# Kernel optimization log

Hardware: AMD Instinct MI355X
Metric: run time of the kernel (lower is better)

The kernel has to match this reference:

```python
import jax, jax.numpy as jnp
from jax import lax
import numpy as np

B, T = 64, 256
PH, POSD, DEPD, DISTD, SDPD = 768, 32, 32, 32, 16
LH, TH, NUM_LABELS = 256, 256, 10
FEAT = PH + POSD + DEPD + 2 * DISTD + SDPD  # 912
TREE_IN = 2 * LH + DEPD                      # 544
D_ITERS = 9  # depth of heads[t]=t//2 tree is 8; 9 sweeps = exact recursion


def setup_inputs() -> dict:
    key = jax.random.key(0)
    ks = jax.random.split(key, 30)
    s = 0.05
    inp = {
        'token_features': jax.random.normal(ks[0], (B, T, PH), jnp.float32),
        'pos_ids': jax.random.randint(ks[1], (B, T), 0, 50),
        'dep_ids': jax.random.randint(ks[2], (B, T), 0, 40),
        'e1_idx': jax.random.randint(ks[3], (B,), 0, T),
        'e2_idx': jax.random.randint(ks[4], (B,), 0, T),
        'sdp_pos': jax.random.randint(ks[5], (B, T), 0, 3),
        'dep_heads': jnp.broadcast_to(jnp.arange(T) // 2, (B, T)),  # root=0 self-loop
        'root_idx': jnp.zeros((B,), jnp.int32),
        # embedding tables
        'pos_table': jax.random.normal(ks[6], (50, POSD)) * s,
        'dep_table': jax.random.normal(ks[7], (40, DEPD)) * s,
        'dist_table': jax.random.normal(ks[8], (21, DISTD)) * s,
        'sdp_table': jax.random.normal(ks[9], (3, SDPD)) * s,
        # feature transform
        'W_ft': jax.random.normal(ks[10], (FEAT, 512)) * s,
        'b_ft': jnp.zeros((512,), jnp.float32),
        # BiLSTM (torch gate order i,f,g,o)
        'Wih_f': jax.random.normal(ks[11], (512, 4 * LH)) * s,
        'Whh_f': jax.random.normal(ks[12], (LH, 4 * LH)) * s,
        'bl_f': jnp.zeros((4 * LH,), jnp.float32),
        'Wih_b': jax.random.normal(ks[13], (512, 4 * LH)) * s,
        'Whh_b': jax.random.normal(ks[14], (LH, 4 * LH)) * s,
        'bl_b': jnp.zeros((4 * LH,), jnp.float32),
        # child-sum TreeLSTM
        'W_iou': jax.random.normal(ks[15], (TREE_IN, 3 * TH)) * s,
        'U_iou': jax.random.normal(ks[16], (TH, 3 * TH)) * s,
        'b_iou': jnp.zeros((3 * TH,), jnp.float32),
        'Wf_t': jax.random.normal(ks[17], (TREE_IN, TH)) * s,
        'Uf_t': jax.random.normal(ks[18], (TH, TH)) * s,
        'bf_t': jnp.zeros((TH,), jnp.float32),
        # classifier
        'W1': jax.random.normal(ks[19], (TH, 256)) * s,
        'b1': jnp.zeros((256,), jnp.float32),
        'W2': jax.random.normal(ks[20], (256, NUM_LABELS)) * s,
        'b2': jnp.zeros((NUM_LABELS,), jnp.float32),
    }
    return inp


def _lstm_dir(x, Wih, Whh, b):
    xW = x @ Wih + b  # [B,T,4H]
    def step(carry, xt):
        h, c = carry
        g = xt + h @ Whh
        i, f, gg, o = jnp.split(g, 4, -1)
        c = jax.nn.sigmoid(f) * c + jax.nn.sigmoid(i) * jnp.tanh(gg)
        h = jax.nn.sigmoid(o) * jnp.tanh(c)
        return (h, c), h
    z = jnp.zeros((x.shape[0], LH), x.dtype)
    _, hs = lax.scan(step, (z, z), jnp.swapaxes(xW, 0, 1))
    return jnp.swapaxes(hs, 0, 1)


def _forward(token_features, pos_table, dep_table, dist_table, sdp_table,
             W_ft, b_ft, Wih_f, Whh_f, bl_f, Wih_b, Whh_b, bl_b,
             W_iou, U_iou, b_iou, Wf_t, Uf_t, bf_t, W1, b1, W2, b2,
             pos_ids, dep_ids, e1_idx, e2_idx, sdp_pos, dep_heads, root_idx):
    pos_emb = pos_table[pos_ids]
    dep_emb = dep_table[dep_ids]
    pos_range = jnp.arange(T)[None, :]
    d1 = jnp.clip(pos_range - e1_idx[:, None] + 10, 0, 20)  # bucket_distance
    d2 = jnp.clip(pos_range - e2_idx[:, None] + 10, 0, 20)
    combined = jnp.concatenate(
        [token_features, pos_emb, dep_emb, dist_table[d1], dist_table[d2], sdp_table[sdp_pos]], -1)
    transformed = jnp.tanh(combined @ W_ft + b_ft)  # [B,T,512] (dropout=eval identity)
    h_f = _lstm_dir(transformed, Wih_f, Whh_f, bl_f)
    h_b = _lstm_dir(transformed[:, ::-1], Wih_b, Whh_b, bl_b)[:, ::-1]
    seq_out = jnp.concatenate([h_f, h_b], -1)           # [B,T,512]
    x_tree = jnp.concatenate([seq_out, dep_emb], -1)    # [B,T,544]
    seg = (dep_heads + jnp.arange(B)[:, None] * T).reshape(-1)
    mask = (dep_heads != pos_range).astype(x_tree.dtype)[..., None]  # drop root self-loop
    xWiou = x_tree @ W_iou + b_iou
    xWf = x_tree @ Wf_t + bf_t
    xWf_par = jnp.take_along_axis(xWf, dep_heads[..., None], axis=1)  # parent's Wf x at each child

    def seg_sum(v):
        return jax.ops.segment_sum(v.reshape(B * T, TH), seg, num_segments=B * T).reshape(B, T, TH)

    def step(carry, _):
        h, c = carry
        h_sum = seg_sum(h * mask)                       # sum of children hidden
        f = jax.nn.sigmoid(xWf_par + h @ Uf_t)          # per-child forget gate
        fc = seg_sum(f * c * mask)
        i, o, u = jnp.split(xWiou + h_sum @ U_iou, 3, -1)
        c2 = jax.nn.sigmoid(i) * jnp.tanh(u) + fc
        h2 = jax.nn.sigmoid(o) * jnp.tanh(c2)
        return (h2, c2), None

    z = jnp.zeros((B, T, TH), x_tree.dtype)
    (h, _), _ = lax.scan(step, (z, z), None, length=D_ITERS)
    root_h = h[jnp.arange(B), root_idx]
    logits = jax.nn.relu(root_h @ W1 + b1) @ W2 + b2
    return logits


def reference(token_features, pos_ids, dep_ids, e1_idx, e2_idx, sdp_pos, dep_heads, root_idx,
              pos_table, dep_table, dist_table, sdp_table, W_ft, b_ft,
              Wih_f, Whh_f, bl_f, Wih_b, Whh_b, bl_b,
              W_iou, U_iou, b_iou, Wf_t, Uf_t, bf_t, W1, b1, W2, b2):
    return _forward(token_features, pos_table, dep_table, dist_table, sdp_table,
                    W_ft, b_ft, Wih_f, Whh_f, bl_f, Wih_b, Whh_b, bl_b,
                    W_iou, U_iou, b_iou, Wf_t, Uf_t, bf_t, W1, b1, W2, b2,
                    pos_ids, dep_ids, e1_idx, e2_idx, sdp_pos, dep_heads, root_idx)
```

## Files before the change

kernel.cpp:

```cpp
#include <hip/hip_runtime.h>
#include <hip/hip_fp16.h>
#include <math.h>


typedef _Float16 f16x8 __attribute__((ext_vector_type(8)));
typedef float    f32x4 __attribute__((ext_vector_type(4)));

union PK1 { _Float16 h; unsigned short u16; };

#define LOG2E 1.44269504088896340736f

__device__ __forceinline__ float fexp2(float x) {
  return __builtin_amdgcn_exp2f(x);
}
__device__ __forceinline__ float frcp(float x) {
  return __builtin_amdgcn_rcpf(x);
}
__device__ __forceinline__ float sigm(float x) {
  return frcp(1.0f + fexp2(-LOG2E * x));
}
__device__ __forceinline__ float tanh_fast(float x) {
  return 1.0f - 2.0f * frcp(1.0f + fexp2(2.0f * LOG2E * x));
}

struct EmbArgs {
  const float* tf; const int* pos_ids; const int* dep_ids;
  const int* e1; const int* e2; const int* sdp;
  const float* pos_tab; const float* dep_tab; const float* dist_tab;
  const float* sdp_tab;
};

__global__ __launch_bounds__(256) void k_prep(
    const float* __restrict__ W_ft, __half* __restrict__ BTft,
    const float* __restrict__ Wih_f, __half* __restrict__ BTwhf,
    const float* __restrict__ Wih_b, __half* __restrict__ BTwhb,
    const float* __restrict__ W_iou, __half* __restrict__ BTiou,
    const float* __restrict__ Wf_t, __half* __restrict__ BTf,
    const float* __restrict__ Whh_f, __half* __restrict__ WBf,
    const float* __restrict__ Whh_b, __half* __restrict__ WBb,
    unsigned int* __restrict__ FLG,
    const int* __restrict__ dep_ids, const float* __restrict__ dep_tab,
    __half* __restrict__ XT,
    const float* __restrict__ Uf, __half* __restrict__ BTuf,
    const float* __restrict__ Uiou, __half* __restrict__ BTuiou) {
  int e = blockIdx.x * 256 + threadIdx.x;
  if (e < 466944) {
    int n = e & 511, k = e >> 9;
    BTft[(size_t)n * 928 + k] = __float2half_rn(W_ft[(size_t)k * 512 + n]);
  } else if ((e -= 466944) < 8192) {
    int n = e >> 4, kk = e & 15;
    BTft[(size_t)n * 928 + 912 + kk] = __float2half_rn(0.0f);
  } else if ((e -= 8192) < 524288) {
    int n = e & 1023, k = e >> 10;
    BTwhf[(size_t)n * 512 + k] = __float2half_rn(Wih_f[(size_t)k * 1024 + n]);
  } else if ((e -= 524288) < 524288) {
    int n = e & 1023, k = e >> 10;
    BTwhb[(size_t)n * 512 + k] = __float2half_rn(Wih_b[(size_t)k * 1024 + n]);
  } else if ((e -= 524288) < 417792) {
    int n = e % 768, k = e / 768;
    BTiou[(size_t)n * 544 + k] = __float2half_rn(W_iou[(size_t)k * 768 + n]);
  } else if ((e -= 417792) < 139264) {
    int n = e & 255, k = e >> 8;
    BTf[(size_t)n * 544 + k] = __float2half_rn(Wf_t[(size_t)k * 256 + n]);
  } else if ((e -= 139264) < 262144) {
    int k = e & 255, c = (e >> 8) & 127, j = e >> 15;
    int col = (c & 3) * 256 + j * 32 + (c >> 2);
    WBf[e] = __float2half_rn(Whh_f[(size_t)k * 1024 + col]);
  } else if ((e -= 262144) < 262144) {
    int k = e & 255, c = (e >> 8) & 127, j = e >> 15;
    int col = (c & 3) * 256 + j * 32 + (c >> 2);
    WBb[e] = __float2half_rn(Whh_b[(size_t)k * 1024 + col]);
  } else if ((e -= 262144) < 32768) {
    FLG[e] = 0u;
  } else if ((e -= 32768) < 524288) {
    int row = e >> 5, kk = e & 31;
    XT[(size_t)row * 544 + 512 + kk] =
        __float2half_rn(dep_tab[dep_ids[row] * 32 + kk]);
  } else if ((e -= 524288) < 65536) {
    int n = e & 255, k = e >> 8;
    BTuf[(size_t)n * 256 + k] = __float2half_rn(Uf[(size_t)k * 256 + n]);
  } else {
    e -= 65536;
    int n = e % 768, k = e / 768;
    BTuiou[(size_t)n * 256 + k] = __float2half_rn(Uiou[(size_t)k * 768 + n]);
  }
}

__global__ __launch_bounds__(256) void k_mgemm(
    const __half* __restrict__ A16, const __half* __restrict__ BT,
    const float* __restrict__ bias, void* __restrict__ out,
    int N, int K, int lda, int a_embed, int act_tanh, int out_mode,
    EmbArgs ea,
    const __half* __restrict__ BT2, const float* __restrict__ bias2,
    void* __restrict__ out2, int N2, int split_bx) {
  __shared__ _Float16 As[128 * 40];
  __shared__ _Float16 Bs[128 * 40];
  int tid = threadIdx.x;
  int lane = tid & 63, wave = tid >> 6;
  int wm = wave & 1, wn = wave >> 1;
  int bxx = blockIdx.x;
  const __half* BTp = BT; const float* biasp = bias;
  void* outp = out; int Np = N;
  if (bxx >= split_bx) {
    bxx -= split_bx; BTp = BT2; biasp = bias2; outp = out2; Np = N2;
  }
  int col0 = bxx * 128, row0 = blockIdx.y * 128;

  f32x4 acc[4][4];
#pragma unroll
  for (int i = 0; i < 4; ++i)
#pragma unroll
    for (int j = 0; j < 4; ++j) acc[i][j] = (f32x4)0.0f;

  for (int kt = 0; kt < K; kt += 32) {
    __syncthreads();
#pragma unroll
    for (int it = 0; it < 2; ++it) {
      int lin = tid + it * 256;
      int r = lin & 127, kh8 = (lin >> 7) * 8;
      f16x8 va;
      if (!a_embed) {
        va = *(const f16x8*)(A16 + (size_t)(row0 + r) * lda + kt + kh8);
      } else {
        int row = row0 + r;
        int k0 = kt + kh8;
        if (k0 >= 912) {
          va = (f16x8)(_Float16)0.0f;
        } else {
          const float* src;
          if (k0 < 768) {
            src = ea.tf + (size_t)row * 768 + k0;
          } else {
            int b_ = row >> 8, t_ = row & 255;
            if (k0 < 800) src = ea.pos_tab + ea.pos_ids[row] * 32 + (k0 - 768);
            else if (k0 < 832) src = ea.dep_tab + ea.dep_ids[row] * 32 + (k0 - 800);
            else if (k0 < 864) {
              int d = t_ - ea.e1[b_] + 10; d = d < 0 ? 0 : (d > 20 ? 20 : d);
              src = ea.dist_tab + d * 32 + (k0 - 832);
            } else if (k0 < 896) {
              int d = t_ - ea.e2[b_] + 10; d = d < 0 ? 0 : (d > 20 ? 20 : d);
              src = ea.dist_tab + d * 32 + (k0 - 864);
            } else {
              src = ea.sdp_tab + ea.sdp[row] * 16 + (k0 - 896);
            }
          }
          float4 a = *(const float4*)src;
          float4 b2 = *(const float4*)(src + 4);
          va[0] = (_Float16)a.x;  va[1] = (_Float16)a.y;
          va[2] = (_Float16)a.z;  va[3] = (_Float16)a.w;
          va[4] = (_Float16)b2.x; va[5] = (_Float16)b2.y;
          va[6] = (_Float16)b2.z; va[7] = (_Float16)b2.w;
        }
      }
      *(f16x8*)&As[r * 40 + kh8] = va;
      f16x8 vb = *(const f16x8*)(BTp + (size_t)(col0 + r) * K + kt + kh8);
      *(f16x8*)&Bs[r * 40 + kh8] = vb;
    }
    __syncthreads();
    f16x8 af[4], bf[4];
    int kq = (lane >> 4) * 8;
#pragma unroll
    for (int mt = 0; mt < 4; ++mt)
      af[mt] = *(const f16x8*)&As[(wm * 64 + mt * 16 + (lane & 15)) * 40 + kq];
#pragma unroll
    for (int nt = 0; nt < 4; ++nt)
      bf[nt] = *(const f16x8*)&Bs[(wn * 64 + nt * 16 + (lane & 15)) * 40 + kq];
#pragma unroll
    for (int mt = 0; mt < 4; ++mt)
#pragma unroll
      for (int nt = 0; nt < 4; ++nt)
        acc[mt][nt] = __builtin_amdgcn_mfma_f32_16x16x32_f16(
            af[mt], bf[nt], acc[mt][nt], 0, 0, 0);
  }

#pragma unroll
  for (int mt = 0; mt < 4; ++mt) {
#pragma unroll
    for (int nt = 0; nt < 4; ++nt) {
      int col = col0 + wn * 64 + nt * 16 + (lane & 15);
      float bv = biasp[col];
#pragma unroll
      for (int r = 0; r < 4; ++r) {
        int row = row0 + wm * 64 + mt * 16 + (lane >> 4) * 4 + r;
        float v = acc[mt][nt][r] + bv;
        if (act_tanh) v = tanh_fast(v);
        if (out_mode == 0) {
          ((float*)outp)[(size_t)row * Np + col] = v;
        } else if (out_mode == 1) {
          ((__half*)outp)[(size_t)row * Np + col] = __float2half_rn(v);
        } else {
          int b_ = row >> 8, t_ = row & 255;
          int g_ = col >> 8, u_ = col & 255;
          int sl = u_ >> 5, ul = u_ & 31;
          ((__half*)outp)[((((size_t)(t_ * 8 + sl) * 4 + g_) * 64 + b_) * 32) + ul] =
              __float2half_rn(v);
        }
      }
    }
  }
}

__global__ __launch_bounds__(256, 1) void k_lstm6(
    const __half* __restrict__ XFs, const __half* __restrict__ XBs,
    const __half* __restrict__ WBf, const __half* __restrict__ WBb,
    __half* __restrict__ HexS, unsigned int* __restrict__ flags,
    __half* __restrict__ XT) {
  int bx = blockIdx.x;
  int dir = bx >> 6, slice = (bx >> 2) & 15, bq = bx & 3;
  int tid = threadIdx.x;
  int lane = tid & 63, wave = tid >> 6;
  const __half* xWs = dir ? XBs : XFs;
  const __half* WB = dir ? WBb : WBf;
  __half* hexd = HexS + (size_t)dir * 256 * 16384;
  unsigned int* flg = flags + (dir * 4 + bq) * 4096;

  __shared__ _Float16 H[16 * 266];
  __shared__ float GT[16 * 69];

  f16x8 bfrag[8];
  {
    int c = (slice & 1) * 64 + wave * 16 + (lane & 15);
#pragma unroll
    for (int kt = 0; kt < 8; ++kt)
      bfrag[kt] = *(const f16x8*)(
          WB + ((size_t)((slice >> 1) * 128 + c) * 256) + kt * 32 +
          (lane >> 4) * 8);
  }
  for (int i = tid; i < 16 * 266 / 8; i += 256)
    ((f16x8*)H)[i] = (f16x8)(_Float16)0.0f;
  float cst = 0.0f;
  int b_own = tid >> 4;
  int uc = tid & 15;
  int bglob = bq * 16 + b_own;
  size_t xw_off = bglob * 32 + (slice & 1) * 16 + uc;
  float xwg[4];
  {
    int t0 = dir ? 255 : 0;
    const __half* xwp = xWs + ((size_t)(t0 * 8 + (slice >> 1)) * 8192) + xw_off;
#pragma unroll
    for (int g = 0; g < 4; ++g) xwg[g] = __half2float(xwp[g * 2048]);
  }
  __syncthreads();

  for (int s = 0; s < 256; ++s) {
    int t = dir ? (255 - s) : s;

    f32x4 acc = (f32x4)0.0f;
#pragma unroll
    for (int kt = 0; kt < 8; ++kt) {
      f16x8 a = *(const f16x8*)&H[(lane & 15) * 266 + kt * 32 +
                                  (lane >> 4) * 8];
      acc = __builtin_amdgcn_mfma_f32_16x16x32_f16(a, bfrag[kt], acc, 0, 0, 0);
    }
    __syncthreads();
    {
      int col = wave * 16 + (lane & 15);
#pragma unroll
      for (int r = 0; r < 4; ++r) {
        int b = (lane >> 4) * 4 + r;
        GT[b * 69 + col] = acc[r];
      }
    }
    __syncthreads();
    float4 g4 = *(const float4*)&GT[b_own * 69 + 4 * uc];
    float gi = g4.x + xwg[0];
    float gf = g4.y + xwg[1];
    float gg = g4.z + xwg[2];
    float go = g4.w + xwg[3];
    cst = sigm(gf) * cst + sigm(gi) * tanh_fast(gg);
    float hn = sigm(go) * tanh_fast(cst);
    PK1 hv; hv.h = (_Float16)hn;
    H[b_own * 266 + slice * 16 + uc] = hv.h;

    if (s < 255) {
      __half* hexq = hexd + (size_t)s * 16384;
      unsigned short* dst =
          (unsigned short*)(hexq + (bq * 16 + slice) * 256 + tid);
      __hip_atomic_store(dst, hv.u16, __ATOMIC_RELAXED,
                         __HIP_MEMORY_SCOPE_AGENT);
      asm volatile("s_waitcnt vmcnt(0)" ::: "memory");
      __syncthreads();
      if (tid == 0)
        __hip_atomic_store(&flg[(slice << 8) + s], 1u, __ATOMIC_RELAXED,
                           __HIP_MEMORY_SCOPE_AGENT);
      XT[(size_t)((bglob << 8) + t) * 544 + dir * 256 + slice * 16 + uc] =
          *(__half*)&hv.h;
      float xwn[4];
      {
        int tn = dir ? (254 - s) : (s + 1);
        const __half* xwp =
            xWs + ((size_t)(tn * 8 + (slice >> 1)) * 8192) + xw_off;
#pragma unroll
        for (int g = 0; g < 4; ++g) xwn[g] = __half2float(xwp[g * 2048]);
      }
      if (tid < 16 && tid != slice) {
        while (__hip_atomic_load(&flg[(tid << 8) + s], __ATOMIC_RELAXED,
                                 __HIP_MEMORY_SCOPE_AGENT) == 0u) {}
      }
      __syncthreads();
#pragma unroll
      for (int i = 0; i < 15; ++i) {
        int ps = i + (i >= slice ? 1 : 0);
        __half pv = hexq[(bq * 16 + ps) * 256 + tid];
        H[b_own * 266 + ps * 16 + uc] = *(_Float16*)&pv;
      }
      __syncthreads();
#pragma unroll
      for (int g = 0; g < 4; ++g) xwg[g] = xwn[g];
    } else {
      XT[(size_t)((bglob << 8) + t) * 544 + dir * 256 + slice * 16 + uc] =
          *(__half*)&hv.h;
    }
  }
}

__global__ __launch_bounds__(256) void k_tgemm(
    const float* __restrict__ A,
    const __half* __restrict__ BT0, float* __restrict__ Cv0, int M0,
    int band_lo0, int blog0,
    const __half* __restrict__ BT1, float* __restrict__ Cv1, int M1,
    int band_lo1, int blog1, int nb0,
    const int* __restrict__ dep_heads,
    const float* __restrict__ xWf, const float* __restrict__ c_buf) {
  __shared__ _Float16 As[128 * 40];
  __shared__ _Float16 Bs[128 * 40];
  int tid = threadIdx.x;
  int lane = tid & 63, wave = tid >> 6;
  int wm = wave & 1, wn = wave >> 1;
  int f = blockIdx.x;
  const __half* BT; float* Cv; int M, N, band_lo, blog, amode, epi;
  int bx, by;
  if (f < nb0) {
    BT = BT0; Cv = Cv0; M = M0; N = 256; band_lo = band_lo0; blog = blog0;
    amode = 1; epi = 2; bx = f & 1; by = f >> 1;
  } else {
    f -= nb0;
    BT = BT1; Cv = Cv1; M = M1; N = 768; band_lo = band_lo1; blog = blog1;
    amode = 2; epi = 0; bx = f % 6; by = f / 6;
  }
  int col0 = bx * 128, row0 = by * 128;
  int bmask = (1 << blog) - 1;

  f32x4 acc[4][4];
#pragma unroll
  for (int i = 0; i < 4; ++i)
#pragma unroll
    for (int j = 0; j < 4; ++j) acc[i][j] = (f32x4)0.0f;

  for (int kt = 0; kt < 256; kt += 32) {
    __syncthreads();
#pragma unroll
    for (int it = 0; it < 2; ++it) {
      int lin = tid + it * 256;
      int r = lin & 127, kh8 = (lin >> 7) * 8;
      int row = row0 + r;
      f16x8 va = (f16x8)(_Float16)0.0f;
      if (row < M) {
        if (amode == 1) {
          int b_ = row >> blog, t_ = band_lo + (row & bmask);
          const float* src = A + (size_t)((b_ << 8) + t_) * 256 + kt + kh8;
          float4 a4 = *(const float4*)src;
          float4 b4 = *(const float4*)(src + 4);
          va[0] = (_Float16)a4.x; va[1] = (_Float16)a4.y;
          va[2] = (_Float16)a4.z; va[3] = (_Float16)a4.w;
          va[4] = (_Float16)b4.x; va[5] = (_Float16)b4.y;
          va[6] = (_Float16)b4.z; va[7] = (_Float16)b4.w;
        } else {
          int b_ = row >> blog, p_ = band_lo + (row & bmask);
          const float* p0 = A + (size_t)((b_ << 8) + 2 * p_) * 256 + kt + kh8;
          float4 x0a = {0.0f, 0.0f, 0.0f, 0.0f};
          float4 x0b = {0.0f, 0.0f, 0.0f, 0.0f};
          if (2 * p_ != 0) {
            x0a = *(const float4*)p0;
            x0b = *(const float4*)(p0 + 4);
          }
          float4 x1a = *(const float4*)(p0 + 256);
          float4 x1b = *(const float4*)(p0 + 260);
          va[0] = (_Float16)(x0a.x + x1a.x); va[1] = (_Float16)(x0a.y + x1a.y);
          va[2] = (_Float16)(x0a.z + x1a.z); va[3] = (_Float16)(x0a.w + x1a.w);
          va[4] = (_Float16)(x0b.x + x1b.x); va[5] = (_Float16)(x0b.y + x1b.y);
          va[6] = (_Float16)(x0b.z + x1b.z); va[7] = (_Float16)(x0b.w + x1b.w);
        }
      }
      *(f16x8*)&As[r * 40 + kh8] = va;
      f16x8 vb = *(const f16x8*)(BT + (size_t)(col0 + r) * 256 + kt + kh8);
      *(f16x8*)&Bs[r * 40 + kh8] = vb;
    }
    __syncthreads();
    f16x8 af[4], bf[4];
    int kq = (lane >> 4) * 8;
#pragma unroll
    for (int mt = 0; mt < 4; ++mt)
      af[mt] = *(const f16x8*)&As[(wm * 64 + mt * 16 + (lane & 15)) * 40 + kq];
#pragma unroll
    for (int nt = 0; nt < 4; ++nt)
      bf[nt] = *(const f16x8*)&Bs[(wn * 64 + nt * 16 + (lane & 15)) * 40 + kq];
#pragma unroll
    for (int mt = 0; mt < 4; ++mt)
#pragma unroll
      for (int nt = 0; nt < 4; ++nt)
        acc[mt][nt] = __builtin_amdgcn_mfma_f32_16x16x32_f16(
            af[mt], bf[nt], acc[mt][nt], 0, 0, 0);
  }

#pragma unroll
  for (int mt = 0; mt < 4; ++mt) {
#pragma unroll
    for (int nt = 0; nt < 4; ++nt) {
      int col = col0 + wn * 64 + nt * 16 + (lane & 15);
#pragma unroll
      for (int r = 0; r < 4; ++r) {
        int row = row0 + wm * 64 + mt * 16 + (lane >> 4) * 4 + r;
        if (row >= M) continue;
        float v = acc[mt][nt][r];
        if (epi == 2) {
          int b_ = row >> blog, t_ = band_lo + (row & bmask);
          int par = dep_heads[(b_ << 8) + t_];
          float m = (par != t_) ? 1.0f : 0.0f;
          float xwv = xWf[(size_t)((b_ << 8) + par) * 256 + col];
          float cv = c_buf[(size_t)((b_ << 8) + t_) * 256 + col];
          v = sigm(v + xwv) * cv * m;
        }
        Cv[(size_t)row * N + col] = v;
      }
    }
  }
}

template <int PLO, int NP>
__device__ __forceinline__ void tree_level(
    int b, int j, float* __restrict__ Hs, float* __restrict__ Cs,
    const float* __restrict__ xWiou, const float* __restrict__ xWf,
    const int* __restrict__ dep_heads,
    const float* __restrict__ Uf, const float* __restrict__ Uiou) {
  constexpr int NCH = 2 * NP;
  constexpr int C0 = 2 * PLO;
  float fd[NCH];
#pragma unroll
  for (int ci = 0; ci < NCH; ++ci) fd[ci] = 0.0f;
  for (int k = 0; k < 256; ++k) {
    float u = Uf[(size_t)k * 256 + j];
#pragma unroll
    for (int ci = 0; ci < NCH; ++ci)
      fd[ci] += Hs[(C0 + ci) * 256 + k] * u;
  }
  float io0[NP], io1[NP], io2[NP];
#pragma unroll
  for (int p = 0; p < NP; ++p) { io0[p] = 0.0f; io1[p] = 0.0f; io2[p] = 0.0f; }
  for (int k = 0; k < 256; ++k) {
    float u0 = Uiou[(size_t)k * 768 + j];
    float u1 = Uiou[(size_t)k * 768 + 256 + j];
    float u2 = Uiou[(size_t)k * 768 + 512 + j];
#pragma unroll
    for (int p = 0; p < NP; ++p) {
      constexpr bool has0 = (PLO != 0);
      int pp = PLO + p;
      float hs = Hs[(2 * pp + 1) * 256 + k];
      if (has0 || p > 0) hs += Hs[2 * pp * 256 + k];
      io0[p] += hs * u0; io1[p] += hs * u1; io2[p] += hs * u2;
    }
  }
  __syncthreads();
#pragma unroll
  for (int p = 0; p < NP; ++p) {
    int pp = PLO + p;
    size_t prow = (size_t)((b << 8) + pp);
    int ta = 2 * pp, tb = 2 * pp + 1;
    int para = dep_heads[(b << 8) + ta];
    int parb = dep_heads[(b << 8) + tb];
    float ma = (para != ta) ? 1.0f : 0.0f;
    float mb = (parb != tb) ? 1.0f : 0.0f;
    float fca = sigm(fd[2 * p] + xWf[(size_t)((b << 8) + para) * 256 + j]) *
                Cs[ta * 256 + j] * ma;
    float fcb = sigm(fd[2 * p + 1] + xWf[(size_t)((b << 8) + parb) * 256 + j]) *
                Cs[tb * 256 + j] * mb;
    float fcsum = fca + fcb;
    float iv = xWiou[prow * 768 + j] + io0[p];
    float ov = xWiou[prow * 768 + 256 + j] + io1[p];
    float uv = xWiou[prow * 768 + 512 + j] + io2[p];
    float cc = sigm(iv) * tanh_fast(uv) + fcsum;
    float hh = sigm(ov) * tanh_fast(cc);
    Cs[pp * 256 + j] = cc;
    Hs[pp * 256 + j] = hh;
  }
  __syncthreads();
}

__global__ __launch_bounds__(256) void k_tree_tail(
    const float* __restrict__ xWiou, const float* __restrict__ xWf,
    const int* __restrict__ dep_heads,
    const float* __restrict__ Uf, const float* __restrict__ Uiou,
    float* __restrict__ h_buf, float* __restrict__ c_buf) {
  int b = blockIdx.x, j = threadIdx.x;
  __shared__ float Hs[32 * 256];
  __shared__ float Cs[32 * 256];
  for (int t = 0; t < 16; ++t) {
    Hs[t * 256 + j] = 0.0f;
    Cs[t * 256 + j] = 0.0f;
  }
  for (int t = 16; t < 32; ++t) {
    size_t row = (size_t)((b << 8) + t);
    Hs[t * 256 + j] = h_buf[row * 256 + j];
    Cs[t * 256 + j] = c_buf[row * 256 + j];
  }
  __syncthreads();
  tree_level<8, 8>(b, j, Hs, Cs, xWiou, xWf, dep_heads, Uf, Uiou);
  tree_level<4, 4>(b, j, Hs, Cs, xWiou, xWf, dep_heads, Uf, Uiou);
  tree_level<2, 2>(b, j, Hs, Cs, xWiou, xWf, dep_heads, Uf, Uiou);
  tree_level<1, 1>(b, j, Hs, Cs, xWiou, xWf, dep_heads, Uf, Uiou);
  tree_level<0, 1>(b, j, Hs, Cs, xWiou, xWf, dep_heads, Uf, Uiou);
  for (int t = 0; t < 16; ++t)
    h_buf[(size_t)((b << 8) + t) * 256 + j] = Hs[t * 256 + j];
}

__global__ __launch_bounds__(256) void k_leaves(
    const float* __restrict__ xWiou, float* __restrict__ h_buf,
    float* __restrict__ c_buf) {
  int r = blockIdx.x;
  int b = r >> 7, t = 128 + (r & 127);
  size_t row = (size_t)((b << 8) + t);
  int j = threadIdx.x;
  float i = xWiou[row * 768 + j];
  float o = xWiou[row * 768 + 256 + j];
  float u = xWiou[row * 768 + 512 + j];
  float c = sigm(i) * tanh_fast(u);
  float h = sigm(o) * tanh_fast(c);
  c_buf[row * 256 + j] = c;
  h_buf[row * 256 + j] = h;
}

__global__ __launch_bounds__(256) void k_update(
    const float* __restrict__ xWiou, const float* __restrict__ iou_lin,
    const float* __restrict__ FC, float* __restrict__ h_buf,
    float* __restrict__ c_buf, int plo, int nplog2) {
  int r = blockIdx.x, j = threadIdx.x;
  int npm = (1 << nplog2) - 1;
  int b = r >> nplog2, loc = r & npm, p = plo + loc;
  size_t row = (size_t)((b << 8) + p);
  float i = xWiou[row * 768 + j] + iou_lin[(size_t)r * 768 + j];
  float o = xWiou[row * 768 + 256 + j] + iou_lin[(size_t)r * 768 + 256 + j];
  float u = xWiou[row * 768 + 512 + j] + iou_lin[(size_t)r * 768 + 512 + j];
  int nch = 2 << nplog2;
  float fc = FC[(size_t)(b * nch + 2 * loc) * 256 + j] +
             FC[(size_t)(b * nch + 2 * loc + 1) * 256 + j];
  float c = sigm(i) * tanh_fast(u) + fc;
  float h = sigm(o) * tanh_fast(c);
  c_buf[row * 256 + j] = c;
  h_buf[row * 256 + j] = h;
}

__global__ __launch_bounds__(256) void k_classifier(
    const float* __restrict__ h_buf, const int* __restrict__ root_idx,
    const float* __restrict__ W1, const float* __restrict__ b1,
    const float* __restrict__ W2, const float* __restrict__ b2,
    float* __restrict__ out) {
  int b = blockIdx.x, j = threadIdx.x;
  __shared__ float hroot[256];
  __shared__ float hid[256];
  int root = root_idx[b];
  hroot[j] = h_buf[(size_t)((b << 8) + root) * 256 + j];
  __syncthreads();
  float acc = b1[j];
  for (int k = 0; k < 256; ++k) acc += hroot[k] * W1[k * 256 + j];
  hid[j] = fmaxf(acc, 0.0f);
  __syncthreads();
  if (j < 10) {
    float o = b2[j];
    for (int k = 0; k < 256; ++k) o += hid[k] * W2[k * 10 + j];
    out[b * 10 + j] = o;
  }
}

extern "C" void kernel_launch(void* const* d_in, const int* in_sizes, int n_in,
                              void* d_out, int out_size, void* d_ws,
                              size_t ws_size, hipStream_t stream) {
  (void)in_sizes; (void)n_in; (void)out_size; (void)ws_size;
  const float* tf       = (const float*)d_in[0];
  const int*   pos_ids  = (const int*)d_in[1];
  const int*   dep_ids  = (const int*)d_in[2];
  const int*   e1       = (const int*)d_in[3];
  const int*   e2       = (const int*)d_in[4];
  const int*   sdp      = (const int*)d_in[5];
  const int*   heads    = (const int*)d_in[6];
  const int*   root     = (const int*)d_in[7];
  const float* pos_tab  = (const float*)d_in[8];
  const float* dep_tab  = (const float*)d_in[9];
  const float* dist_tab = (const float*)d_in[10];
  const float* sdp_tab  = (const float*)d_in[11];
  const float* W_ft     = (const float*)d_in[12];
  const float* b_ft     = (const float*)d_in[13];
  const float* Wih_f    = (const float*)d_in[14];
  const float* Whh_f    = (const float*)d_in[15];
  const float* bl_f     = (const float*)d_in[16];
  const float* Wih_b    = (const float*)d_in[17];
  const float* Whh_b    = (const float*)d_in[18];
  const float* bl_b     = (const float*)d_in[19];
  const float* W_iou    = (const float*)d_in[20];
  const float* U_iou    = (const float*)d_in[21];
  const float* b_iou    = (const float*)d_in[22];
  const float* Wf_t     = (const float*)d_in[23];
  const float* Uf_t     = (const float*)d_in[24];
  const float* bf_t     = (const float*)d_in[25];
  const float* W1       = (const float*)d_in[26];
  const float* b1       = (const float*)d_in[27];
  const float* W2       = (const float*)d_in[28];
  const float* b2       = (const float*)d_in[29];

  char* ws = (char*)d_ws;
  __half* XF    = (__half*)(ws + 0ull);
  __half* XB    = (__half*)(ws + 33554432ull);
  float*  XWIOU = (float*)(ws + 0ull);
  float*  XWF   = (float*)(ws + 50331648ull);
  __half* XT    = (__half*)(ws + 67108864ull);
  float*  FCb   = (float*)(ws + 67108864ull);
  float*  IOUL  = (float*)(ws + 75497472ull);
  float*  H     = (float*)(ws + 88080384ull);
  __half* T     = (__half*)(ws + 88080384ull);
  __half* HexS  = (__half*)(ws + 88080384ull);
  float*  C     = (float*)(ws + 104857600ull);
  __half* BTft  = (__half*)(ws + 104857600ull);
  __half* BTwhf = (__half*)(ws + 105807872ull);
  __half* BTwhb = (__half*)(ws + 106856448ull);
  __half* BTiou = (__half*)(ws + 107905024ull);
  __half* BTf   = (__half*)(ws + 108740608ull);
  __half* WBf   = (__half*)(ws + 109019136ull);
  __half* WBb   = (__half*)(ws + 109543424ull);
  unsigned int* FLG = (unsigned int*)(ws + 110198784ull);
  __half* BTuiou = (__half*)(ws + 121634816ull);
  __half* BTuf   = (__half*)(ws + 122028032ull);

  EmbArgs ea{tf, pos_ids, dep_ids, e1, e2, sdp, pos_tab, dep_tab, dist_tab, sdp_tab};

  k_prep<<<dim3(13376), dim3(256), 0, stream>>>(
      W_ft, BTft, Wih_f, BTwhf, Wih_b, BTwhb, W_iou, BTiou, Wf_t, BTf,
      Whh_f, WBf, Whh_b, WBb, FLG, dep_ids, dep_tab, XT,
      Uf_t, BTuf, U_iou, BTuiou);

  k_mgemm<<<dim3(4, 128), dim3(256), 0, stream>>>(
      nullptr, BTft, b_ft, (void*)T, 512, 928, 0, 1, 1, 1, ea,
      BTft, b_ft, (void*)T, 512, 10000);
  k_mgemm<<<dim3(16, 128), dim3(256), 0, stream>>>(
      T, BTwhf, bl_f, (void*)XF, 1024, 512, 512, 0, 0, 2, ea,
      BTwhb, bl_b, (void*)XB, 1024, 8);
  k_lstm6<<<dim3(128), dim3(256), 0, stream>>>(XF, XB, WBf, WBb, HexS, FLG, XT);
  k_mgemm<<<dim3(8, 128), dim3(256), 0, stream>>>(
      XT, BTiou, b_iou, (void*)XWIOU, 768, 544, 544, 0, 0, 0, ea,
      BTf, bf_t, (void*)XWF, 256, 6);
  k_leaves<<<dim3(8192), dim3(256), 0, stream>>>(XWIOU, H, C);
  const int plos[3] = {64, 32, 16};
  const int lgs[3]  = {6, 5, 4};
  for (int s = 0; s < 3; ++s) {
    int plo = plos[s], lg = lgs[s];
    int npar = 1 << lg;
    int Mch = 128 * npar;
    int Mp = 64 * npar;
    int nb0 = 2 * npar;
    int nb1 = 6 * ((Mp + 127) / 128);
    k_tgemm<<<dim3(nb0 + nb1), dim3(256), 0, stream>>>(
        H, BTuf, FCb, Mch, 2 * plo, lg + 1,
        BTuiou, IOUL, Mp, plo, lg, nb0, heads, XWF, C);
    k_update<<<dim3(Mp), dim3(256), 0, stream>>>(XWIOU, IOUL, FCb, H, C, plo, lg);
  }
  k_tree_tail<<<dim3(64), dim3(256), 0, stream>>>(XWIOU, XWF, heads,
                                                  Uf_t, U_iou, H, C);
  k_classifier<<<dim3(64), dim3(256), 0, stream>>>(H, root, W1, b1, W2, b2,
                                                   (float*)d_out);
}
```

Before: 1.153 ms.

## Split LSTM recurrence across 256 blocks with 8 batches each

The recurrent BiLSTM kernel now uses 256 blocks instead of 128, and each block handles 8 batch rows instead of 16. Half the MFMA rows are padding that the valid mask ignores, and the flag array and prep-kernel zeroing are doubled to cover 8 batch groups. One barrier before the gate-tile write is removed. The intent is to spread the latency-bound recurrence across more CUs, which doubles the cross-block flag traffic and wastes half of each MFMA tile.

```diff
diff --git a/kernel.cpp b/kernel.cpp
--- a/kernel.cpp
+++ b/kernel.cpp
@@ -70,9 +70,9 @@
     int k = e & 255, c = (e >> 8) & 127, j = e >> 15;
     int col = (c & 3) * 256 + j * 32 + (c >> 2);
     WBb[e] = __float2half_rn(Whh_b[(size_t)k * 1024 + col]);
-  } else if ((e -= 262144) < 32768) {
+  } else if ((e -= 262144) < 65536) {
     FLG[e] = 0u;
-  } else if ((e -= 32768) < 524288) {
+  } else if ((e -= 65536) < 524288) {
     int row = e >> 5, kk = e & 31;
     XT[(size_t)row * 544 + 512 + kk] =
         __float2half_rn(dep_tab[dep_ids[row] * 32 + kk]);
@@ -200,19 +200,19 @@
   }
 }
 
-__global__ __launch_bounds__(256, 1) void k_lstm6(
+__global__ __launch_bounds__(256, 1) void k_lstm7(
     const __half* __restrict__ XFs, const __half* __restrict__ XBs,
     const __half* __restrict__ WBf, const __half* __restrict__ WBb,
     __half* __restrict__ HexS, unsigned int* __restrict__ flags,
     __half* __restrict__ XT) {
   int bx = blockIdx.x;
-  int dir = bx >> 6, slice = (bx >> 2) & 15, bq = bx & 3;
+  int dir = bx >> 7, slice = (bx >> 3) & 15, be = bx & 7;
   int tid = threadIdx.x;
   int lane = tid & 63, wave = tid >> 6;
   const __half* xWs = dir ? XBs : XFs;
   const __half* WB = dir ? WBb : WBf;
   __half* hexd = HexS + (size_t)dir * 256 * 16384;
-  unsigned int* flg = flags + (dir * 4 + bq) * 4096;
+  unsigned int* flg = flags + (dir * 8 + be) * 4096;
 
   __shared__ _Float16 H[16 * 266];
   __shared__ float GT[16 * 69];
@@ -231,10 +231,11 @@
   float cst = 0.0f;
   int b_own = tid >> 4;
   int uc = tid & 15;
-  int bglob = bq * 16 + b_own;
-  size_t xw_off = bglob * 32 + (slice & 1) * 16 + uc;
-  float xwg[4];
-  {
+  bool valid = (b_own < 8);
+  int bglob = be * 8 + b_own;
+  size_t xw_off = (size_t)bglob * 32 + (slice & 1) * 16 + uc;
+  float xwg[4] = {0.0f, 0.0f, 0.0f, 0.0f};
+  if (valid) {
     int t0 = dir ? 255 : 0;
     const __half* xwp = xWs + ((size_t)(t0 * 8 + (slice >> 1)) * 8192) + xw_off;
 #pragma unroll
@@ -252,7 +253,6 @@
                                   (lane >> 4) * 8];
       acc = __builtin_amdgcn_mfma_f32_16x16x32_f16(a, bfrag[kt], acc, 0, 0, 0);
     }
-    __syncthreads();
     {
       int col = wave * 16 + (lane & 15);
 #pragma unroll
@@ -262,31 +262,37 @@
       }
     }
     __syncthreads();
-    float4 g4 = *(const float4*)&GT[b_own * 69 + 4 * uc];
-    float gi = g4.x + xwg[0];
-    float gf = g4.y + xwg[1];
-    float gg = g4.z + xwg[2];
-    float go = g4.w + xwg[3];
-    cst = sigm(gf) * cst + sigm(gi) * tanh_fast(gg);
-    float hn = sigm(go) * tanh_fast(cst);
-    PK1 hv; hv.h = (_Float16)hn;
-    H[b_own * 266 + slice * 16 + uc] = hv.h;
+    PK1 hv; hv.u16 = 0;
+    if (valid) {
+      float4 g4 = *(const float4*)&GT[b_own * 69 + 4 * uc];
+      float gi = g4.x + xwg[0];
+      float gf = g4.y + xwg[1];
+      float gg = g4.z + xwg[2];
+      float go = g4.w + xwg[3];
+      cst = sigm(gf) * cst + sigm(gi) * tanh_fast(gg);
+      float hn = sigm(go) * tanh_fast(cst);
+      hv.h = (_Float16)hn;
+      H[b_own * 266 + slice * 16 + uc] = hv.h;
+    }
 
     if (s < 255) {
       __half* hexq = hexd + (size_t)s * 16384;
-      unsigned short* dst =
-          (unsigned short*)(hexq + (bq * 16 + slice) * 256 + tid);
-      __hip_atomic_store(dst, hv.u16, __ATOMIC_RELAXED,
-                         __HIP_MEMORY_SCOPE_AGENT);
+      if (valid) {
+        unsigned short* dst =
+            (unsigned short*)(hexq + (be * 16 + slice) * 128 + tid);
+        __hip_atomic_store(dst, hv.u16, __ATOMIC_RELAXED,
+                           __HIP_MEMORY_SCOPE_AGENT);
+      }
       asm volatile("s_waitcnt vmcnt(0)" ::: "memory");
       __syncthreads();
       if (tid == 0)
         __hip_atomic_store(&flg[(slice << 8) + s], 1u, __ATOMIC_RELAXED,
                            __HIP_MEMORY_SCOPE_AGENT);
-      XT[(size_t)((bglob << 8) + t) * 544 + dir * 256 + slice * 16 + uc] =
-          *(__half*)&hv.h;
-      float xwn[4];
-      {
+      if (valid)
+        XT[(size_t)((bglob << 8) + t) * 544 + dir * 256 + slice * 16 + uc] =
+            *(__half*)&hv.h;
+      float xwn[4] = {0.0f, 0.0f, 0.0f, 0.0f};
+      if (valid) {
         int tn = dir ? (254 - s) : (s + 1);
         const __half* xwp =
             xWs + ((size_t)(tn * 8 + (slice >> 1)) * 8192) + xw_off;
@@ -298,18 +304,21 @@
                                  __HIP_MEMORY_SCOPE_AGENT) == 0u) {}
       }
       __syncthreads();
-#pragma unroll
-      for (int i = 0; i < 15; ++i) {
-        int ps = i + (i >= slice ? 1 : 0);
-        __half pv = hexq[(bq * 16 + ps) * 256 + tid];
-        H[b_own * 266 + ps * 16 + uc] = *(_Float16*)&pv;
+      if (valid) {
+#pragma unroll
+        for (int i = 0; i < 15; ++i) {
+          int ps = i + (i >= slice ? 1 : 0);
+          __half pv = hexq[(be * 16 + ps) * 128 + tid];
+          H[b_own * 266 + ps * 16 + uc] = *(_Float16*)&pv;
+        }
       }
       __syncthreads();
 #pragma unroll
       for (int g = 0; g < 4; ++g) xwg[g] = xwn[g];
     } else {
-      XT[(size_t)((bglob << 8) + t) * 544 + dir * 256 + slice * 16 + uc] =
-          *(__half*)&hv.h;
+      if (valid)
+        XT[(size_t)((bglob << 8) + t) * 544 + dir * 256 + slice * 16 + uc] =
+            *(__half*)&hv.h;
     }
   }
 }
@@ -631,7 +640,7 @@
 
   EmbArgs ea{tf, pos_ids, dep_ids, e1, e2, sdp, pos_tab, dep_tab, dist_tab, sdp_tab};
 
-  k_prep<<<dim3(13376), dim3(256), 0, stream>>>(
+  k_prep<<<dim3(13504), dim3(256), 0, stream>>>(
       W_ft, BTft, Wih_f, BTwhf, Wih_b, BTwhb, W_iou, BTiou, Wf_t, BTf,
       Whh_f, WBf, Whh_b, WBb, FLG, dep_ids, dep_tab, XT,
       Uf_t, BTuf, U_iou, BTuiou);
@@ -642,7 +651,7 @@
   k_mgemm<<<dim3(16, 128), dim3(256), 0, stream>>>(
       T, BTwhf, bl_f, (void*)XF, 1024, 512, 512, 0, 0, 2, ea,
       BTwhb, bl_b, (void*)XB, 1024, 8);
-  k_lstm6<<<dim3(128), dim3(256), 0, stream>>>(XF, XB, WBf, WBb, HexS, FLG, XT);
+  k_lstm7<<<dim3(256), dim3(256), 0, stream>>>(XF, XB, WBf, WBb, HexS, FLG, XT);
   k_mgemm<<<dim3(8, 128), dim3(256), 0, stream>>>(
       XT, BTiou, b_iou, (void*)XWIOU, 768, 544, 544, 0, 0, 0, ea,
       BTf, bf_t, (void*)XWF, 256, 6);
```

Result: no change. 1.140 ms (-1.1%).
